# Kernel tuning notes

Hardware: AMD Instinct MI355X
Metric: run time of the kernel (lower is better)

Reference implementation:

```python
import jax, jax.numpy as jnp
import numpy as np

D_MODEL = 1024
NUM_HEADS = 16
HEAD_DIM = D_MODEL // NUM_HEADS


def setup_inputs() -> dict:
    key = jax.random.key(0)
    ks = jax.random.split(key, 9)
    B, S = 4, 2048
    scale = 1.0 / np.sqrt(D_MODEL)
    x = jax.random.normal(ks[0], (B, S, D_MODEL), dtype=jnp.float32)
    Wq = jax.random.normal(ks[1], (D_MODEL, D_MODEL), dtype=jnp.float32) * scale
    bq = jnp.zeros((D_MODEL,), dtype=jnp.float32)
    Wk = jax.random.normal(ks[2], (D_MODEL, D_MODEL), dtype=jnp.float32) * scale
    bk = jnp.zeros((D_MODEL,), dtype=jnp.float32)
    Wv = jax.random.normal(ks[3], (D_MODEL, D_MODEL), dtype=jnp.float32) * scale
    bv = jnp.zeros((D_MODEL,), dtype=jnp.float32)
    Wo = jax.random.normal(ks[4], (D_MODEL, D_MODEL), dtype=jnp.float32) * scale
    bo = jnp.zeros((D_MODEL,), dtype=jnp.float32)
    return {"x": x, "Wq": Wq, "bq": bq, "Wk": Wk, "bk": bk,
            "Wv": Wv, "bv": bv, "Wo": Wo, "bo": bo}


def reference(x, Wq, bq, Wk, bk, Wv, bv, Wo, bo):
    B, S, D = x.shape
    H, Hd = NUM_HEADS, HEAD_DIM
    # linear projections then split heads: [B,S,D] -> [B,H,S,Hd]
    def split(t):
        return t.reshape(B, S, H, Hd).transpose(0, 2, 1, 3)
    q = split(x @ Wq + bq)
    k = split(x @ Wk + bk)
    v = split(x @ Wv + bv)
    scores = jnp.einsum('bhsd,bhtd->bhst', q, k) / jnp.sqrt(
        jnp.asarray(Hd, dtype=jnp.float32))
    attn = jax.nn.softmax(scores, axis=-1)
    out = jnp.einsum('bhst,bhtd->bhsd', attn, v)  # [B,H,S,Hd]
    out = out.transpose(0, 2, 1, 3).reshape(B, S, D)
    return out @ Wo + bo
```

## Files before the change

kernel.cpp:

```cpp
#include <hip/hip_runtime.h>

#define DM 1024
#define NH 16
#define HD 64
#define SEQ 2048
#define BATCH 4
#define MROWS (BATCH*SEQ)

typedef short short8 __attribute__((ext_vector_type(8)));
typedef float f32x4 __attribute__((ext_vector_type(4)));
typedef unsigned short u16x8 __attribute__((ext_vector_type(8)));
typedef unsigned short u16x4 __attribute__((ext_vector_type(4)));

__device__ inline unsigned short f2b(float f) {
    union { float f; unsigned u; } v; v.f = f;
    unsigned r = v.u + 0x7fffu + ((v.u >> 16) & 1u);
    return (unsigned short)(r >> 16);
}

__device__ inline void gload_lds16(const void* g, void* l) {
    __builtin_amdgcn_global_load_lds(
        (const __attribute__((address_space(1))) void*)g,
        (__attribute__((address_space(3))) void*)l, 16, 0, 0);
}

__device__ inline unsigned cvt_pk_bf16(float lo, float hi) {
    unsigned r;
    asm("v_cvt_pk_bf16_f32 %0, %1, %2" : "=v"(r) : "v"(lo), "v"(hi));
    return r;
}

__global__ void k_cvt_x(const float* __restrict__ x, unsigned short* __restrict__ xb) {
    long i = ((long)blockIdx.x * 256 + threadIdx.x) * 8;
    float4 a = *reinterpret_cast<const float4*>(x + i);
    float4 b = *reinterpret_cast<const float4*>(x + i + 4);
    u16x8 o;
    o[0]=f2b(a.x); o[1]=f2b(a.y); o[2]=f2b(a.z); o[3]=f2b(a.w);
    o[4]=f2b(b.x); o[5]=f2b(b.y); o[6]=f2b(b.z); o[7]=f2b(b.w);
    *reinterpret_cast<u16x8*>(xb + i) = o;
}

__global__ void k_cvt_wT(const float* W0, const float* W1, const float* W2, const float* W3,
                         unsigned short* __restrict__ out) {
    const float* Ws[4] = {W0, W1, W2, W3};
    const float* W = Ws[blockIdx.z];
    unsigned short* o = out + (size_t)blockIdx.z * DM * DM;
    __shared__ float t[64][65];
    int tx = threadIdx.x & 15, ty = threadIdx.x >> 4;
    int nb = blockIdx.x * 64, kb = blockIdx.y * 64;
#pragma unroll
    for (int i = 0; i < 4; ++i) {
        int r = ty + 16 * i;
        float4 v = *reinterpret_cast<const float4*>(W + (size_t)(kb + r) * DM + nb + tx * 4);
        t[r][tx*4+0] = v.x; t[r][tx*4+1] = v.y; t[r][tx*4+2] = v.z; t[r][tx*4+3] = v.w;
    }
    __syncthreads();
#pragma unroll
    for (int i = 0; i < 4; ++i) {
        int r = ty + 16 * i;
        u16x4 pv;
#pragma unroll
        for (int j = 0; j < 4; ++j) pv[j] = f2b(t[tx*4+j][r]);
        *reinterpret_cast<u16x4*>(o + (size_t)(nb + r) * DM + kb + tx * 4) = pv;
    }
}

#define BM 128
#define BN 128
#define BK 64
#define QSCALE 0.1803368801f

__global__ __launch_bounds__(256) void k_gemm(const unsigned short* __restrict__ A,
                                              const unsigned short* __restrict__ Bt,
                                              const float* __restrict__ bias,
                                              unsigned short* __restrict__ outb,
                                              float* __restrict__ outf, int mode) {
    __shared__ unsigned short lds[BM*BK + BN*BK];
    unsigned short* lA = lds;
    unsigned short* lB = lds + BM*BK;
    int tid = threadIdx.x, lane = tid & 63, wv = tid >> 6;
    int wr = wv >> 1, wc = wv & 1;
    int c = lane & 15, g = lane >> 4;
    int m0 = blockIdx.x * BM, n0 = blockIdx.y * BN;
    f32x4 acc[4][4] = {};

    for (int kt = 0; kt < DM / BK; ++kt) {
#pragma unroll
        for (int it = 0; it < 4; ++it) {
            int sgi = it * 256 + tid;
            int row = sgi >> 3, blk = sgi & 7;
            int srcoff = kt * BK + ((blk ^ (row & 7)) << 3);
            gload_lds16(A  + (size_t)(m0 + row) * DM + srcoff, &lA[(it*256 + wv*64) * 8]);
            gload_lds16(Bt + (size_t)(n0 + row) * DM + srcoff, &lB[(it*256 + wv*64) * 8]);
        }
        __syncthreads();
#pragma unroll
        for (int ks = 0; ks < 2; ++ks) {
            short8 af[4], bf[4];
#pragma unroll
            for (int mi = 0; mi < 4; ++mi) {
                int row = wr*64 + mi*16 + c;
                af[mi] = *reinterpret_cast<const short8*>(&lA[row*64 + (((ks*4 + g) ^ (row & 7)) << 3)]);
            }
#pragma unroll
            for (int ni = 0; ni < 4; ++ni) {
                int row = wc*64 + ni*16 + c;
                bf[ni] = *reinterpret_cast<const short8*>(&lB[row*64 + (((ks*4 + g) ^ (row & 7)) << 3)]);
            }
#pragma unroll
            for (int mi = 0; mi < 4; ++mi)
#pragma unroll
                for (int ni = 0; ni < 4; ++ni)
                    acc[mi][ni] = __builtin_amdgcn_mfma_f32_16x16x32_bf16(af[mi], bf[ni], acc[mi][ni], 0, 0, 0);
        }
        __syncthreads();
    }

    if (mode <= 1) {
        float sc = (mode == 0) ? QSCALE : 1.0f;
#pragma unroll
        for (int mi = 0; mi < 4; ++mi)
#pragma unroll
            for (int ni = 0; ni < 4; ++ni)
#pragma unroll
                for (int r = 0; r < 4; ++r) {
                    int gr = m0 + wr*64 + mi*16 + 4*g + r;
                    int gc = n0 + wc*64 + ni*16 + c;
                    float v = (acc[mi][ni][r] + bias[gc]) * sc;
                    int b = gr >> 11, s = gr & 2047, h = gc >> 6, d = gc & 63;
                    outb[(((size_t)(b*NH + h) * SEQ + s) << 6) + d] = f2b(v);
                }
    } else if (mode == 2) {
        unsigned short* t = lds;
#pragma unroll
        for (int mi = 0; mi < 4; ++mi)
#pragma unroll
            for (int ni = 0; ni < 4; ++ni)
#pragma unroll
                for (int r = 0; r < 4; ++r) {
                    int lr = wr*64 + mi*16 + 4*g + r;
                    int lc = wc*64 + ni*16 + c;
                    t[lc*128 + lr] = f2b(acc[mi][ni][r] + bias[n0 + lc]);
                }
        __syncthreads();
#pragma unroll
        for (int i = 0; i < 8; ++i) {
            int idx = (i*256 + tid) * 8;
            int lc = idx >> 7, lr = idx & 127;
            int gcol = n0 + lc, grow = m0 + lr;
            int b = grow >> 11, s = grow & 2047, h = gcol >> 6, d = gcol & 63;
            *reinterpret_cast<u16x8*>(&outb[((size_t)((b*NH + h) << 6) + d) * SEQ + s]) =
                *reinterpret_cast<u16x8*>(&t[idx]);
        }
    } else {
#pragma unroll
        for (int mi = 0; mi < 4; ++mi)
#pragma unroll
            for (int ni = 0; ni < 4; ++ni)
#pragma unroll
                for (int r = 0; r < 4; ++r) {
                    int gr = m0 + wr*64 + mi*16 + 4*g + r;
                    int gc = n0 + wc*64 + ni*16 + c;
                    outf[(size_t)gr * DM + gc] = acc[mi][ni][r] + bias[gc];
                }
    }
}

__global__ __launch_bounds__(256) void k_attn(const unsigned short* __restrict__ Q,
                                              const unsigned short* __restrict__ K,
                                              const unsigned short* __restrict__ VT,
                                              unsigned short* __restrict__ AO) {
    __shared__ unsigned short kt[2][64*64], vt[2][64*64];
    int tid = threadIdx.x, lane = tid & 63, wv = tid >> 6;
    int c = lane & 15, g = lane >> 4;

    int flat = blockIdx.x;
    int nb = (flat & 7) * 256 + (flat >> 3);
    int qb = nb & 31, bh = nb >> 5;

    const unsigned short* Qh = Q  + (size_t)bh * SEQ * HD;
    const unsigned short* Kh = K  + (size_t)bh * SEQ * HD;
    const unsigned short* Vh = VT + (size_t)bh * HD * SEQ;

    int qrow = qb*64 + wv*16 + c;
    short8 qf[2];
    qf[0] = *reinterpret_cast<const short8*>(&Qh[(size_t)qrow*HD +      g*8]);
    qf[1] = *reinterpret_cast<const short8*>(&Qh[(size_t)qrow*HD + 32 + g*8]);

    float m = -1e30f, l = 0.f;
    f32x4 oacc[4] = {};

    auto stage = [&](int buf, int t) {
#pragma unroll
        for (int it = 0; it < 2; ++it) {
            int sgi = it*256 + tid;
            int row = sgi >> 3, blk = sgi & 7;
            int srow = ((row >> 4) & 1)*32 + ((row >> 2) & 3)*8 + ((row >> 5) & 1)*4 + (row & 3);
            gload_lds16(Kh + (size_t)(t*64 + srow)*HD + ((blk ^ (row & 7)) << 3),
                        &kt[buf][(it*256 + wv*64) * 8]);
            gload_lds16(Vh + (size_t)row*SEQ + t*64 + ((blk ^ (row & 7)) << 3),
                        &vt[buf][(it*256 + wv*64) * 8]);
        }
    };

    stage(0, 0);
    __syncthreads();

    int cur = 0;
    for (int t = 0; t < SEQ/64; ++t) {
        if (t + 1 < SEQ/64) stage(cur ^ 1, t + 1);

        f32x4 sacc[4] = {};
        __builtin_amdgcn_s_setprio(1);
#pragma unroll
        for (int ks = 0; ks < 2; ++ks)
#pragma unroll
            for (int nt = 0; nt < 4; ++nt) {
                int y = nt*16 + c;
                short8 kf = *reinterpret_cast<const short8*>(
                    &kt[cur][y*64 + (((ks*4 + g) ^ (y & 7)) << 3)]);
                sacc[nt] = __builtin_amdgcn_mfma_f32_16x16x32_bf16(kf, qf[ks], sacc[nt], 0, 0, 0);
            }
        __builtin_amdgcn_s_setprio(0);

        float t0 = fmaxf(fmaxf(sacc[0][0], sacc[0][1]), fmaxf(sacc[0][2], sacc[0][3]));
        float t1 = fmaxf(fmaxf(sacc[1][0], sacc[1][1]), fmaxf(sacc[1][2], sacc[1][3]));
        float t2 = fmaxf(fmaxf(sacc[2][0], sacc[2][1]), fmaxf(sacc[2][2], sacc[2][3]));
        float t3 = fmaxf(fmaxf(sacc[3][0], sacc[3][1]), fmaxf(sacc[3][2], sacc[3][3]));
        float tm = fmaxf(fmaxf(t0, t1), fmaxf(t2, t3));
        tm = fmaxf(tm, __shfl_xor(tm, 16, 64));
        tm = fmaxf(tm, __shfl_xor(tm, 32, 64));

        if (!__all(tm <= m + 8.0f)) {
            float mn = fmaxf(m, tm);
            float corr = __builtin_amdgcn_exp2f(m - mn);
            m = mn;
            l *= corr;
#pragma unroll
            for (int ft = 0; ft < 4; ++ft)
#pragma unroll
                for (int r = 0; r < 4; ++r) oacc[ft][r] *= corr;
        }

        float s0 = 0.f, s1 = 0.f, s2 = 0.f, s3 = 0.f;
#pragma unroll
        for (int r = 0; r < 4; ++r) {
            float p0 = __builtin_amdgcn_exp2f(sacc[0][r] - m);
            float p1 = __builtin_amdgcn_exp2f(sacc[1][r] - m);
            float p2 = __builtin_amdgcn_exp2f(sacc[2][r] - m);
            float p3 = __builtin_amdgcn_exp2f(sacc[3][r] - m);
            sacc[0][r] = p0; sacc[1][r] = p1; sacc[2][r] = p2; sacc[3][r] = p3;
            s0 += p0; s1 += p1; s2 += p2; s3 += p3;
        }
        float s = (s0 + s1) + (s2 + s3);
        s += __shfl_xor(s, 16, 64);
        s += __shfl_xor(s, 32, 64);
        l += s;

        union { unsigned u[4]; short8 v; } U0, U1;
        U0.u[0] = cvt_pk_bf16(sacc[0][0], sacc[0][1]);
        U0.u[1] = cvt_pk_bf16(sacc[0][2], sacc[0][3]);
        U0.u[2] = cvt_pk_bf16(sacc[2][0], sacc[2][1]);
        U0.u[3] = cvt_pk_bf16(sacc[2][2], sacc[2][3]);
        U1.u[0] = cvt_pk_bf16(sacc[1][0], sacc[1][1]);
        U1.u[1] = cvt_pk_bf16(sacc[1][2], sacc[1][3]);
        U1.u[2] = cvt_pk_bf16(sacc[3][0], sacc[3][1]);
        U1.u[3] = cvt_pk_bf16(sacc[3][2], sacc[3][3]);
        short8 pa0 = U0.v, pa1 = U1.v;

        __builtin_amdgcn_s_setprio(1);
#pragma unroll
        for (int ft = 0; ft < 4; ++ft) {
            int y = ft*16 + c;
            short8 vf0 = *reinterpret_cast<const short8*>(
                &vt[cur][y*64 + ((g ^ (y & 7)) << 3)]);
            short8 vf1 = *reinterpret_cast<const short8*>(
                &vt[cur][y*64 + (((4 + g) ^ (y & 7)) << 3)]);
            oacc[ft] = __builtin_amdgcn_mfma_f32_16x16x32_bf16(vf0, pa0, oacc[ft], 0, 0, 0);
            oacc[ft] = __builtin_amdgcn_mfma_f32_16x16x32_bf16(vf1, pa1, oacc[ft], 0, 0, 0);
        }
        __builtin_amdgcn_s_setprio(0);

        __syncthreads();
        cur ^= 1;
    }

    int b = bh >> 4, h = bh & 15;
    float inv = 1.f / l;
#pragma unroll
    for (int ft = 0; ft < 4; ++ft) {
        u16x4 o4;
#pragma unroll
        for (int r = 0; r < 4; ++r) o4[r] = f2b(oacc[ft][r] * inv);
        *reinterpret_cast<u16x4*>(
            &AO[(size_t)(b*SEQ + qrow) * DM + h*HD + ft*16 + 4*g]) = o4;
    }
}

extern "C" void kernel_launch(void* const* d_in, const int* in_sizes, int n_in,
                              void* d_out, int out_size, void* d_ws, size_t ws_size,
                              hipStream_t stream) {
    const float* x  = (const float*)d_in[0];
    const float* Wq = (const float*)d_in[1];
    const float* bq = (const float*)d_in[2];
    const float* Wk = (const float*)d_in[3];
    const float* bk = (const float*)d_in[4];
    const float* Wv = (const float*)d_in[5];
    const float* bv = (const float*)d_in[6];
    const float* Wo = (const float*)d_in[7];
    const float* bo = (const float*)d_in[8];

    char* ws = (char*)d_ws;
    unsigned short* xb  = (unsigned short*)(ws);
    unsigned short* wT  = (unsigned short*)(ws + (16u<<20));
    unsigned short* Qb  = (unsigned short*)(ws + (24u<<20));
    unsigned short* Kb  = (unsigned short*)(ws + (40u<<20));
    unsigned short* VTb = (unsigned short*)(ws + (56u<<20));
    unsigned short* AOb = (unsigned short*)(ws + (72u<<20));

    k_cvt_x<<<dim3(MROWS*DM/8/256), 256, 0, stream>>>(x, xb);
    k_cvt_wT<<<dim3(16,16,4), 256, 0, stream>>>(Wq, Wk, Wv, Wo, wT);

    k_gemm<<<dim3(MROWS/BM, DM/BN), 256, 0, stream>>>(xb, wT,            bq, Qb,  nullptr, 0);
    k_gemm<<<dim3(MROWS/BM, DM/BN), 256, 0, stream>>>(xb, wT + DM*DM,    bk, Kb,  nullptr, 1);
    k_gemm<<<dim3(MROWS/BM, DM/BN), 256, 0, stream>>>(xb, wT + 2*DM*DM,  bv, VTb, nullptr, 2);

    k_attn<<<dim3(SEQ/64 * BATCH*NH), 256, 0, stream>>>(Qb, Kb, VTb, AOb);

    k_gemm<<<dim3(MROWS/BM, DM/BN), 256, 0, stream>>>(AOb, wT + 3*DM*DM, bo, nullptr, (float*)d_out, 3);
}
```

Before: 228.3 us.

## Deepen attention K/V pipeline to four stages and compute row sums via MFMA

```diff
diff --git a/kernel.cpp b/kernel.cpp
--- a/kernel.cpp
+++ b/kernel.cpp
@@ -170,7 +170,7 @@
                                               const unsigned short* __restrict__ K,
                                               const unsigned short* __restrict__ VT,
                                               unsigned short* __restrict__ AO) {
-    __shared__ unsigned short kt[2][64*64], vt[2][64*64];
+    __shared__ unsigned short kt[4][64*64], vt[4][64*64];
     int tid = threadIdx.x, lane = tid & 63, wv = tid >> 6;
     int c = lane & 15, g = lane >> 4;
 
@@ -187,28 +187,38 @@
     qf[0] = *reinterpret_cast<const short8*>(&Qh[(size_t)qrow*HD +      g*8]);
     qf[1] = *reinterpret_cast<const short8*>(&Qh[(size_t)qrow*HD + 32 + g*8]);
 
-    float m = -1e30f, l = 0.f;
-    f32x4 oacc[4] = {};
+    int row = tid >> 3, blk = tid & 7;
+    int xo = (blk ^ (row & 7)) << 3;
+    auto srow = [](int r) {
+        return ((r >> 4) & 1)*32 + ((r >> 2) & 3)*8 + ((r >> 5) & 1)*4 + (r & 3);
+    };
+    const unsigned short* gK0 = Kh + (size_t)srow(row)      * HD + xo;
+    const unsigned short* gK1 = Kh + (size_t)srow(row + 32) * HD + xo;
+    const unsigned short* gV0 = Vh + (size_t)row        * SEQ + xo;
+    const unsigned short* gV1 = Vh + (size_t)(row + 32) * SEQ + xo;
+    unsigned ldso = wv * 512;
 
     auto stage = [&](int buf, int t) {
-#pragma unroll
-        for (int it = 0; it < 2; ++it) {
-            int sgi = it*256 + tid;
-            int row = sgi >> 3, blk = sgi & 7;
-            int srow = ((row >> 4) & 1)*32 + ((row >> 2) & 3)*8 + ((row >> 5) & 1)*4 + (row & 3);
-            gload_lds16(Kh + (size_t)(t*64 + srow)*HD + ((blk ^ (row & 7)) << 3),
-                        &kt[buf][(it*256 + wv*64) * 8]);
-            gload_lds16(Vh + (size_t)row*SEQ + t*64 + ((blk ^ (row & 7)) << 3),
-                        &vt[buf][(it*256 + wv*64) * 8]);
-        }
+        gload_lds16(gK0 + (size_t)t*64*HD, &kt[buf][ldso]);
+        gload_lds16(gK1 + (size_t)t*64*HD, &kt[buf][2048 + ldso]);
+        gload_lds16(gV0 + t*64,            &vt[buf][ldso]);
+        gload_lds16(gV1 + t*64,            &vt[buf][2048 + ldso]);
     };
 
-    stage(0, 0);
-    __syncthreads();
-
-    int cur = 0;
+    float m = -1e30f;
+    f32x4 oacc[4] = {}, lacc = {};
+    const short ob = (short)0x3F80;
+    const short8 ones = {ob, ob, ob, ob, ob, ob, ob, ob};
+
+    stage(0, 0); stage(1, 1); stage(2, 2);
+
     for (int t = 0; t < SEQ/64; ++t) {
-        if (t + 1 < SEQ/64) stage(cur ^ 1, t + 1);
+        if (t <= 29)      asm volatile("s_waitcnt vmcnt(8)" ::: "memory");
+        else if (t == 30) asm volatile("s_waitcnt vmcnt(4)" ::: "memory");
+        else              asm volatile("s_waitcnt vmcnt(0)" ::: "memory");
+        __builtin_amdgcn_s_barrier();
+        if (t + 3 < SEQ/64) stage((t + 3) & 3, t + 3);
+        int cur = t & 3;
 
         f32x4 sacc[4] = {};
         __builtin_amdgcn_s_setprio(1);
@@ -228,34 +238,25 @@
         float t2 = fmaxf(fmaxf(sacc[2][0], sacc[2][1]), fmaxf(sacc[2][2], sacc[2][3]));
         float t3 = fmaxf(fmaxf(sacc[3][0], sacc[3][1]), fmaxf(sacc[3][2], sacc[3][3]));
         float tm = fmaxf(fmaxf(t0, t1), fmaxf(t2, t3));
-        tm = fmaxf(tm, __shfl_xor(tm, 16, 64));
-        tm = fmaxf(tm, __shfl_xor(tm, 32, 64));
-
-        if (!__all(tm <= m + 8.0f)) {
+
+        if (__any(tm > m + 8.0f)) {
+            tm = fmaxf(tm, __shfl_xor(tm, 16, 64));
+            tm = fmaxf(tm, __shfl_xor(tm, 32, 64));
             float mn = fmaxf(m, tm);
             float corr = __builtin_amdgcn_exp2f(m - mn);
             m = mn;
-            l *= corr;
+            lacc *= corr;
 #pragma unroll
             for (int ft = 0; ft < 4; ++ft)
 #pragma unroll
                 for (int r = 0; r < 4; ++r) oacc[ft][r] *= corr;
         }
 
-        float s0 = 0.f, s1 = 0.f, s2 = 0.f, s3 = 0.f;
-#pragma unroll
-        for (int r = 0; r < 4; ++r) {
-            float p0 = __builtin_amdgcn_exp2f(sacc[0][r] - m);
-            float p1 = __builtin_amdgcn_exp2f(sacc[1][r] - m);
-            float p2 = __builtin_amdgcn_exp2f(sacc[2][r] - m);
-            float p3 = __builtin_amdgcn_exp2f(sacc[3][r] - m);
-            sacc[0][r] = p0; sacc[1][r] = p1; sacc[2][r] = p2; sacc[3][r] = p3;
-            s0 += p0; s1 += p1; s2 += p2; s3 += p3;
-        }
-        float s = (s0 + s1) + (s2 + s3);
-        s += __shfl_xor(s, 16, 64);
-        s += __shfl_xor(s, 32, 64);
-        l += s;
+#pragma unroll
+        for (int nt = 0; nt < 4; ++nt)
+#pragma unroll
+            for (int r = 0; r < 4; ++r)
+                sacc[nt][r] = __builtin_amdgcn_exp2f(sacc[nt][r] - m);
 
         union { unsigned u[4]; short8 v; } U0, U1;
         U0.u[0] = cvt_pk_bf16(sacc[0][0], sacc[0][1]);
@@ -279,14 +280,13 @@
             oacc[ft] = __builtin_amdgcn_mfma_f32_16x16x32_bf16(vf0, pa0, oacc[ft], 0, 0, 0);
             oacc[ft] = __builtin_amdgcn_mfma_f32_16x16x32_bf16(vf1, pa1, oacc[ft], 0, 0, 0);
         }
+        lacc = __builtin_amdgcn_mfma_f32_16x16x32_bf16(ones, pa0, lacc, 0, 0, 0);
+        lacc = __builtin_amdgcn_mfma_f32_16x16x32_bf16(ones, pa1, lacc, 0, 0, 0);
         __builtin_amdgcn_s_setprio(0);
-
-        __syncthreads();
-        cur ^= 1;
     }
 
     int b = bh >> 4, h = bh & 15;
-    float inv = 1.f / l;
+    float inv = 1.f / lacc[0];
 #pragma unroll
     for (int ft = 0; ft < 4; ++ft) {
         u16x4 o4;
```

Measured after the change: 249.6 us. +9.3%, slower.
